# Kernel tuning notes

Measured on AMD Instinct MI355X. Metric: run time of the kernel, lower is better.

The kernel has to match this reference:

```python
import math
import jax, jax.numpy as jnp
import numpy as np


def _sinkhorn_attn(q, n):
    """Log-domain Sinkhorn-Knopp, eps=1, max_iter=1, uniform marginals.
    cost C = -q @ q^T, so M = (-C + u + v)/eps = S + u + v with S = q q^T.
    Returns transport plan pi = exp(S + u_i + v_j).  q: [B, n, d]."""
    S = jnp.einsum('bnd,bmd->bnm', q, q)            # [B, n, n]
    log_marg = -math.log(n)                          # log(1/n)
    u = log_marg - jax.nn.logsumexp(S, axis=-1)      # [B, n] row update
    v = log_marg - jax.nn.logsumexp(S + u[..., :, None], axis=-2)  # [B, n] col update
    return jnp.exp(S + u[..., :, None] + v[..., None, :])


def reference(x, row_embed, col_embed):
    # x: [B, d, H, W]; row_embed/col_embed: [len_embedding, d//2]
    B, d, H, W = x.shape
    # learned positional embedding: [H, W, d] -> [d, H, W]
    x_emb = col_embed[:W]                             # [W, F]
    y_emb = row_embed[:H]                             # [H, F]
    F = x_emb.shape[-1]
    pos = jnp.concatenate([
        jnp.broadcast_to(x_emb[None, :, :], (H, W, F)),
        jnp.broadcast_to(y_emb[:, None, :], (H, W, F)),
    ], axis=-1).transpose(2, 0, 1)                    # [d, H, W]
    x = x + pos[None]

    n = H * W
    xf = x.reshape(B, d, n).transpose(0, 2, 1)        # [B, n, d] = q = k = v (v unscaled)
    inv_sqrtV = 1.0 / math.sqrt(math.sqrt(d))         # d**-0.25 applied to q and k each
    attn = _sinkhorn_attn(xf * inv_sqrtV, n)          # [B, n, n]
    out = jnp.einsum('bnm,bmd->bnd', attn, xf)        # [B, n, d]
    return out.transpose(0, 2, 1).reshape(B, d, H, W)


def setup_inputs() -> dict:
    key = jax.random.key(0)
    k1, k2, k3 = jax.random.split(key, 3)
    B, d, H, W = 32, 512, 32, 32
    len_emb, F = 32, d // 2
    return {
        'x': jax.random.normal(k1, (B, d, H, W), dtype=jnp.float32),
        'row_embed': jax.random.uniform(k2, (len_emb, F), dtype=jnp.float32),
        'col_embed': jax.random.uniform(k3, (len_emb, F), dtype=jnp.float32),
    }
```

## Files before the change

kernel.cpp:

```cpp
#include <hip/hip_runtime.h>
#include <hip/hip_fp16.h>
#include <math.h>

typedef _Float16 f16;
typedef _Float16 f16x8 __attribute__((ext_vector_type(8)));
typedef _Float16 f16x4 __attribute__((ext_vector_type(4)));
typedef float f32x4 __attribute__((ext_vector_type(4)));

namespace {
constexpr int kB = 32, kD = 512, kN = 1024, kF = 256;
constexpr float kScale = 0.04419417382415922f;
constexpr float kLogMarg = -6.931471805599453f;
constexpr float kMarg = 1.f / 1024.f;
constexpr float kPScale = 16384.f;
constexpr float kPInv = 1.f / 16384.f;
constexpr int LDK = 72;
}

__global__ __launch_bounds__(256) void k_prep(
    const float* __restrict__ x, const float* __restrict__ re,
    const float* __restrict__ ce, f16* __restrict__ xf,
    f16* __restrict__ xfT, int b0) {
  __shared__ f16 T[64][68];
  const int lb = blockIdx.z;
  const int i0 = blockIdx.x * 64, c0 = blockIdx.y * 64;
  const int t = threadIdx.x;
  const int il = (t & 15) * 4;
  const int cl = t >> 4;
  const size_t xbase = ((size_t)(b0 + lb) * kD) * kN;
#pragma unroll
  for (int p = 0; p < 4; p++) {
    const int c = c0 + cl + 16 * p;
    const int i = i0 + il;
    const float4 xv = *(const float4*)(x + xbase + (size_t)c * kN + i);
    float4 pv;
    if (c < kF) {
      pv.x = ce[((i + 0) & 31) * kF + c];
      pv.y = ce[((i + 1) & 31) * kF + c];
      pv.z = ce[((i + 2) & 31) * kF + c];
      pv.w = ce[((i + 3) & 31) * kF + c];
    } else {
      const float r = re[(i >> 5) * kF + (c - kF)];
      pv.x = r; pv.y = r; pv.z = r; pv.w = r;
    }
    const f16 h0 = (f16)(xv.x + pv.x), h1 = (f16)(xv.y + pv.y);
    const f16 h2 = (f16)(xv.z + pv.z), h3 = (f16)(xv.w + pv.w);
    f16* dT = xfT + ((size_t)lb * kD + c) * kN + i;
    *(f16x4*)dT = (f16x4){h0, h1, h2, h3};
    T[cl + 16 * p][il + 0] = h0; T[cl + 16 * p][il + 1] = h1;
    T[cl + 16 * p][il + 2] = h2; T[cl + 16 * p][il + 3] = h3;
  }
  __syncthreads();
#pragma unroll
  for (int p = 0; p < 4; p++) {
    const int ir = cl + 16 * p;
    const int cc = il;
    const f16 h0 = T[cc + 0][ir], h1 = T[cc + 1][ir];
    const f16 h2 = T[cc + 2][ir], h3 = T[cc + 3][ir];
    f16* dF = xf + ((size_t)lb * kN + i0 + ir) * kD + c0 + cc;
    *(f16x4*)dF = (f16x4){h0, h1, h2, h3};
  }
}

__global__ __launch_bounds__(256) void k_gemm_s(
    const f16* __restrict__ xf, f16* __restrict__ S16,
    float* __restrict__ rp) {
  __shared__ f16 As[128][LDK];
  __shared__ f16 Bs[128][LDK];
  const int lb = blockIdx.z;
  const int i0 = blockIdx.y * 128, j0 = blockIdx.x * 128;
  const f16* base = xf + (size_t)lb * kN * kD;
  const int t = threadIdx.x;
  const int w = t >> 6, lane = t & 63;
  const int m_off = (w >> 1) * 64, n_off = (w & 1) * 64;
  const int quad = lane >> 4, l15 = lane & 15;
  const int sc = (t & 7) * 8;
  const int sr = t >> 3;
  f32x4 acc[4][4];
#pragma unroll
  for (int a = 0; a < 4; a++)
#pragma unroll
    for (int b = 0; b < 4; b++) acc[a][b] = (f32x4){0.f, 0.f, 0.f, 0.f};

  for (int k0 = 0; k0 < kD; k0 += 64) {
    f16x8 a[4], b[4];
#pragma unroll
    for (int p = 0; p < 4; p++) {
      a[p] = *(const f16x8*)(base + (size_t)(i0 + sr + 32 * p) * kD + k0 + sc);
      b[p] = *(const f16x8*)(base + (size_t)(j0 + sr + 32 * p) * kD + k0 + sc);
    }
    __syncthreads();
#pragma unroll
    for (int p = 0; p < 4; p++) {
      *(f16x8*)&As[sr + 32 * p][sc] = a[p];
      *(f16x8*)&Bs[sr + 32 * p][sc] = b[p];
    }
    __syncthreads();
#pragma unroll
    for (int kk = 0; kk < 64; kk += 32) {
      f16x8 af[4], bf[4];
#pragma unroll
      for (int q = 0; q < 4; q++)
        af[q] = *(const f16x8*)&As[m_off + 16 * q + l15][kk + quad * 8];
#pragma unroll
      for (int q = 0; q < 4; q++)
        bf[q] = *(const f16x8*)&Bs[n_off + 16 * q + l15][kk + quad * 8];
#pragma unroll
      for (int qa = 0; qa < 4; qa++)
#pragma unroll
        for (int qb = 0; qb < 4; qb++)
          acc[qa][qb] = __builtin_amdgcn_mfma_f32_16x16x32_f16(
              af[qa], bf[qb], acc[qa][qb], 0, 0, 0);
    }
  }
  f16* Sb = S16 + (size_t)lb * kN * kN;
  const int jt2 = blockIdx.x * 2 + (w & 1);
  float* rpb = rp + ((size_t)lb * 16 + jt2) * kN + i0 + m_off;
#pragma unroll
  for (int qa = 0; qa < 4; qa++) {
    const int i = i0 + m_off + 16 * qa + quad * 4;
    float rs[4] = {0.f, 0.f, 0.f, 0.f};
#pragma unroll
    for (int qb = 0; qb < 4; qb++) {
      const int j = j0 + n_off + 16 * qb + l15;
#pragma unroll
      for (int r = 0; r < 4; r++) {
        const f16 h = (f16)(acc[qa][qb][r] * kScale);
        Sb[(size_t)(i + r) * kN + j] = h;
        rs[r] += __expf((float)h);
      }
    }
#pragma unroll
    for (int r = 0; r < 4; r++) {
      float s = rs[r];
      s += __shfl_xor(s, 1);
      s += __shfl_xor(s, 2);
      s += __shfl_xor(s, 4);
      s += __shfl_xor(s, 8);
      if (l15 == 0) rpb[16 * qa + 4 * quad + r] = s;
    }
  }
}

__global__ __launch_bounds__(256) void k_u(
    const float* __restrict__ rp, float* __restrict__ u) {
  const int lb = blockIdx.y;
  const int i = blockIdx.x * 256 + threadIdx.x;
  const float* r = rp + (size_t)lb * 16 * kN + i;
  float s = 0.f;
#pragma unroll
  for (int t = 0; t < 16; t++) s += r[(size_t)t * kN];
  u[lb * kN + i] = kLogMarg - __logf(s);
}

__global__ __launch_bounds__(256) void k_cs(
    const f16* __restrict__ S16, const float* __restrict__ u,
    float* __restrict__ cp) {
  const int lb = blockIdx.z;
  const int seg = blockIdx.y;
  const int j = blockIdx.x * 256 + threadIdx.x;
  const f16* Sb = S16 + (size_t)lb * kN * kN + j;
  const float* ub = u + lb * kN + seg * 64;
  const size_t rbase = (size_t)(seg * 64) * kN;
  float s = 0.f;
#pragma unroll 4
  for (int r = 0; r < 64; r++)
    s += __expf((float)Sb[rbase + (size_t)r * kN] + ub[r]);
  cp[((size_t)lb * 16 + seg) * kN + j] = s;
}

__global__ __launch_bounds__(256) void k_v(
    const float* __restrict__ cp, float* __restrict__ ev) {
  const int lb = blockIdx.y;
  const int j = blockIdx.x * 256 + threadIdx.x;
  const float* c = cp + (size_t)lb * 16 * kN + j;
  float s = 0.f;
#pragma unroll
  for (int r = 0; r < 16; r++) s += c[(size_t)r * kN];
  ev[lb * kN + j] = kMarg / s;
}

__global__ __launch_bounds__(256) void k_pt(
    const f16* __restrict__ S16, const float* __restrict__ u,
    const float* __restrict__ ev, f16* __restrict__ t16) {
  const int row = blockIdx.x;
  const float ui = u[row];
  const f16* Sr = S16 + (size_t)row * kN;
  const float* evb = ev + (size_t)(row >> 10) * kN;
  f16* Tr = t16 + (size_t)row * kN;
  const int j = threadIdx.x * 4;
  const f16x4 s = *(const f16x4*)(Sr + j);
  const float4 e = *(const float4*)(evb + j);
  f16x4 o;
  o[0] = (f16)(__expf((float)s[0] + ui) * e.x * kPScale);
  o[1] = (f16)(__expf((float)s[1] + ui) * e.y * kPScale);
  o[2] = (f16)(__expf((float)s[2] + ui) * e.z * kPScale);
  o[3] = (f16)(__expf((float)s[3] + ui) * e.w * kPScale);
  *(f16x4*)(Tr + j) = o;
}

__global__ __launch_bounds__(256) void k_gemm_o(
    const f16* __restrict__ xfT, const f16* __restrict__ P,
    float* __restrict__ out, int b0) {
  __shared__ f16 As[128][LDK];
  __shared__ f16 Bs[128][LDK];
  const int lb = blockIdx.z;
  const int i0 = blockIdx.x * 128, c0 = blockIdx.y * 128;
  const f16* Ab = xfT + (size_t)lb * kD * kN;
  const f16* Bb = P + (size_t)lb * kN * kN;
  const int t = threadIdx.x;
  const int w = t >> 6, lane = t & 63;
  const int m_off = (w >> 1) * 64, n_off = (w & 1) * 64;
  const int quad = lane >> 4, l15 = lane & 15;
  const int sc = (t & 7) * 8;
  const int sr = t >> 3;
  f32x4 acc[4][4];
#pragma unroll
  for (int a = 0; a < 4; a++)
#pragma unroll
    for (int b = 0; b < 4; b++) acc[a][b] = (f32x4){0.f, 0.f, 0.f, 0.f};

  for (int k0 = 0; k0 < kN; k0 += 64) {
    f16x8 a[4], b[4];
#pragma unroll
    for (int p = 0; p < 4; p++) {
      a[p] = *(const f16x8*)(Ab + (size_t)(c0 + sr + 32 * p) * kN + k0 + sc);
      b[p] = *(const f16x8*)(Bb + (size_t)(i0 + sr + 32 * p) * kN + k0 + sc);
    }
    __syncthreads();
#pragma unroll
    for (int p = 0; p < 4; p++) {
      *(f16x8*)&As[sr + 32 * p][sc] = a[p];
      *(f16x8*)&Bs[sr + 32 * p][sc] = b[p];
    }
    __syncthreads();
#pragma unroll
    for (int kk = 0; kk < 64; kk += 32) {
      f16x8 af[4], bf[4];
#pragma unroll
      for (int q = 0; q < 4; q++)
        af[q] = *(const f16x8*)&As[m_off + 16 * q + l15][kk + quad * 8];
#pragma unroll
      for (int q = 0; q < 4; q++)
        bf[q] = *(const f16x8*)&Bs[n_off + 16 * q + l15][kk + quad * 8];
#pragma unroll
      for (int qa = 0; qa < 4; qa++)
#pragma unroll
        for (int qb = 0; qb < 4; qb++)
          acc[qa][qb] = __builtin_amdgcn_mfma_f32_16x16x32_f16(
              af[qa], bf[qb], acc[qa][qb], 0, 0, 0);
    }
  }
  float* ob = out + ((size_t)(b0 + lb) * kD) * kN;
#pragma unroll
  for (int qa = 0; qa < 4; qa++) {
    const int c = c0 + m_off + 16 * qa + quad * 4;
#pragma unroll
    for (int qb = 0; qb < 4; qb++) {
      const int i = i0 + n_off + 16 * qb + l15;
#pragma unroll
      for (int r = 0; r < 4; r++)
        ob[(size_t)(c + r) * kN + i] = acc[qa][qb][r] * kPInv;
    }
  }
}

extern "C" void kernel_launch(void* const* d_in, const int* in_sizes, int n_in,
                              void* d_out, int out_size, void* d_ws, size_t ws_size,
                              hipStream_t stream) {
  const float* x = (const float*)d_in[0];
  const float* re = (const float*)d_in[1];
  const float* ce = (const float*)d_in[2];
  float* out = (float*)d_out;

  char* wsb = (char*)d_ws;
  const size_t perb = 2097152ull + 1048576 + 1048576 + 2097152 +
                      4096 + 4096 + 65536 + 65536;
  int G = (int)(ws_size / perb);
  if (G >= 32) G = 32;
  else if (G >= 16) G = 16;
  else if (G >= 8) G = 8;
  else if (G >= 4) G = 4;
  else if (G < 1) G = 1;
  f16* S16 = (f16*)wsb;
  f16* xf = (f16*)(wsb + (size_t)G * 2097152);
  f16* xfT = (f16*)((char*)xf + (size_t)G * 1048576);
  f16* t16 = (f16*)((char*)xfT + (size_t)G * 1048576);
  float* u = (float*)((char*)t16 + (size_t)G * 2097152);
  float* ev = u + (size_t)G * kN;
  float* rp = ev + (size_t)G * kN;
  float* cp = rp + (size_t)G * 16 * kN;

  for (int b0 = 0; b0 < kB; b0 += G) {
    const int g = (kB - b0 < G) ? (kB - b0) : G;
    k_prep<<<dim3(16, 8, g), 256, 0, stream>>>(x, re, ce, xf, xfT, b0);
    k_gemm_s<<<dim3(8, 8, g), 256, 0, stream>>>(xf, S16, rp);
    k_u<<<dim3(4, g), 256, 0, stream>>>(rp, u);
    k_cs<<<dim3(4, 16, g), 256, 0, stream>>>(S16, u, cp);
    k_v<<<dim3(4, g), 256, 0, stream>>>(cp, ev);
    k_pt<<<g * kN, 256, 0, stream>>>(S16, u, ev, t16);
    k_gemm_o<<<dim3(8, 4, g), 256, 0, stream>>>(xfT, t16, out, b0);
  }
}
```

Before: 286.3 us.

## Load GEMM tiles directly into LDS with global_load_lds and XOR swizzle

Both GEMM kernels now fetch their A and B tiles straight from global memory into shared memory with the global_load_lds builtin. This bypasses the VGPR staging and separate LDS stores. The padded shared layout becomes a dense 128-byte row layout with an XOR swizzle on the 16-byte chunk index, applied to the source address and undone on the fragment reads, to avoid bank conflicts. The barrier after compute is kept, but loads are still not double-buffered, so load latency is not overlapped with MFMA work. The code relies on the wave-uniform LDS base plus per-lane 16-byte placement matching the precomputed swizzled source offsets.

```diff
diff --git a/kernel.cpp b/kernel.cpp
--- a/kernel.cpp
+++ b/kernel.cpp
@@ -14,7 +14,12 @@
 constexpr float kMarg = 1.f / 1024.f;
 constexpr float kPScale = 16384.f;
 constexpr float kPInv = 1.f / 16384.f;
-constexpr int LDK = 72;
+}
+
+__device__ __forceinline__ void gload16(const void* g, void* l) {
+  __builtin_amdgcn_global_load_lds(
+      (const __attribute__((address_space(1))) void*)g,
+      (__attribute__((address_space(3))) void*)l, 16, 0, 0);
 }
 
 __global__ __launch_bounds__(256) void k_prep(
@@ -65,46 +70,52 @@
 __global__ __launch_bounds__(256) void k_gemm_s(
     const f16* __restrict__ xf, f16* __restrict__ S16,
     float* __restrict__ rp) {
-  __shared__ f16 As[128][LDK];
-  __shared__ f16 Bs[128][LDK];
+  __shared__ char sm[32768];
   const int lb = blockIdx.z;
   const int i0 = blockIdx.y * 128, j0 = blockIdx.x * 128;
-  const f16* base = xf + (size_t)lb * kN * kD;
+  const char* base = (const char*)(xf + (size_t)lb * kN * kD);
   const int t = threadIdx.x;
   const int w = t >> 6, lane = t & 63;
   const int m_off = (w >> 1) * 64, n_off = (w & 1) * 64;
   const int quad = lane >> 4, l15 = lane & 15;
-  const int sc = (t & 7) * 8;
-  const int sr = t >> 3;
+  const int swz = (l15 & 7) << 4;
+
+  int srcA[4], srcB[4], ldsw[4];
+#pragma unroll
+  for (int p = 0; p < 4; p++) {
+    const int off = p * 4096 + w * 1024 + lane * 16;
+    const int r = off >> 7;
+    const int cb = (off & 127) ^ ((r & 7) << 4);
+    srcA[p] = (i0 + r) * (kD * 2) + cb;
+    srcB[p] = (j0 + r) * (kD * 2) + cb;
+    ldsw[p] = p * 4096 + w * 1024;
+  }
+
   f32x4 acc[4][4];
 #pragma unroll
   for (int a = 0; a < 4; a++)
 #pragma unroll
     for (int b = 0; b < 4; b++) acc[a][b] = (f32x4){0.f, 0.f, 0.f, 0.f};
 
-  for (int k0 = 0; k0 < kD; k0 += 64) {
-    f16x8 a[4], b[4];
-#pragma unroll
-    for (int p = 0; p < 4; p++) {
-      a[p] = *(const f16x8*)(base + (size_t)(i0 + sr + 32 * p) * kD + k0 + sc);
-      b[p] = *(const f16x8*)(base + (size_t)(j0 + sr + 32 * p) * kD + k0 + sc);
-    }
+  for (int k0b = 0; k0b < kD * 2; k0b += 128) {
+#pragma unroll
+    for (int p = 0; p < 4; p++)
+      gload16(base + srcA[p] + k0b, sm + ldsw[p]);
+#pragma unroll
+    for (int p = 0; p < 4; p++)
+      gload16(base + srcB[p] + k0b, sm + 16384 + ldsw[p]);
     __syncthreads();
 #pragma unroll
-    for (int p = 0; p < 4; p++) {
-      *(f16x8*)&As[sr + 32 * p][sc] = a[p];
-      *(f16x8*)&Bs[sr + 32 * p][sc] = b[p];
-    }
-    __syncthreads();
-#pragma unroll
-    for (int kk = 0; kk < 64; kk += 32) {
+    for (int kk = 0; kk < 2; kk++) {
       f16x8 af[4], bf[4];
 #pragma unroll
       for (int q = 0; q < 4; q++)
-        af[q] = *(const f16x8*)&As[m_off + 16 * q + l15][kk + quad * 8];
+        af[q] = *(const f16x8*)(sm + (m_off + 16 * q + l15) * 128 +
+                                ((kk * 64 + quad * 16) ^ swz));
 #pragma unroll
       for (int q = 0; q < 4; q++)
-        bf[q] = *(const f16x8*)&Bs[n_off + 16 * q + l15][kk + quad * 8];
+        bf[q] = *(const f16x8*)(sm + 16384 + (n_off + 16 * q + l15) * 128 +
+                                ((kk * 64 + quad * 16) ^ swz));
 #pragma unroll
       for (int qa = 0; qa < 4; qa++)
 #pragma unroll
@@ -112,7 +123,9 @@
           acc[qa][qb] = __builtin_amdgcn_mfma_f32_16x16x32_f16(
               af[qa], bf[qb], acc[qa][qb], 0, 0, 0);
     }
-  }
+    __syncthreads();
+  }
+
   f16* Sb = S16 + (size_t)lb * kN * kN;
   const int jt2 = blockIdx.x * 2 + (w & 1);
   float* rpb = rp + ((size_t)lb * 16 + jt2) * kN + i0 + m_off;
@@ -202,47 +215,53 @@
 __global__ __launch_bounds__(256) void k_gemm_o(
     const f16* __restrict__ xfT, const f16* __restrict__ P,
     float* __restrict__ out, int b0) {
-  __shared__ f16 As[128][LDK];
-  __shared__ f16 Bs[128][LDK];
+  __shared__ char sm[32768];
   const int lb = blockIdx.z;
   const int i0 = blockIdx.x * 128, c0 = blockIdx.y * 128;
-  const f16* Ab = xfT + (size_t)lb * kD * kN;
-  const f16* Bb = P + (size_t)lb * kN * kN;
+  const char* Ab = (const char*)(xfT + (size_t)lb * kD * kN);
+  const char* Bb = (const char*)(P + (size_t)lb * kN * kN);
   const int t = threadIdx.x;
   const int w = t >> 6, lane = t & 63;
   const int m_off = (w >> 1) * 64, n_off = (w & 1) * 64;
   const int quad = lane >> 4, l15 = lane & 15;
-  const int sc = (t & 7) * 8;
-  const int sr = t >> 3;
+  const int swz = (l15 & 7) << 4;
+
+  int srcA[4], srcB[4], ldsw[4];
+#pragma unroll
+  for (int p = 0; p < 4; p++) {
+    const int off = p * 4096 + w * 1024 + lane * 16;
+    const int r = off >> 7;
+    const int cb = (off & 127) ^ ((r & 7) << 4);
+    srcA[p] = (c0 + r) * (kN * 2) + cb;
+    srcB[p] = (i0 + r) * (kN * 2) + cb;
+    ldsw[p] = p * 4096 + w * 1024;
+  }
+
   f32x4 acc[4][4];
 #pragma unroll
   for (int a = 0; a < 4; a++)
 #pragma unroll
     for (int b = 0; b < 4; b++) acc[a][b] = (f32x4){0.f, 0.f, 0.f, 0.f};
 
-  for (int k0 = 0; k0 < kN; k0 += 64) {
-    f16x8 a[4], b[4];
-#pragma unroll
-    for (int p = 0; p < 4; p++) {
-      a[p] = *(const f16x8*)(Ab + (size_t)(c0 + sr + 32 * p) * kN + k0 + sc);
-      b[p] = *(const f16x8*)(Bb + (size_t)(i0 + sr + 32 * p) * kN + k0 + sc);
-    }
+  for (int k0b = 0; k0b < kN * 2; k0b += 128) {
+#pragma unroll
+    for (int p = 0; p < 4; p++)
+      gload16(Ab + srcA[p] + k0b, sm + ldsw[p]);
+#pragma unroll
+    for (int p = 0; p < 4; p++)
+      gload16(Bb + srcB[p] + k0b, sm + 16384 + ldsw[p]);
     __syncthreads();
 #pragma unroll
-    for (int p = 0; p < 4; p++) {
-      *(f16x8*)&As[sr + 32 * p][sc] = a[p];
-      *(f16x8*)&Bs[sr + 32 * p][sc] = b[p];
-    }
-    __syncthreads();
-#pragma unroll
-    for (int kk = 0; kk < 64; kk += 32) {
+    for (int kk = 0; kk < 2; kk++) {
       f16x8 af[4], bf[4];
 #pragma unroll
       for (int q = 0; q < 4; q++)
-        af[q] = *(const f16x8*)&As[m_off + 16 * q + l15][kk + quad * 8];
+        af[q] = *(const f16x8*)(sm + (m_off + 16 * q + l15) * 128 +
+                                ((kk * 64 + quad * 16) ^ swz));
 #pragma unroll
       for (int q = 0; q < 4; q++)
-        bf[q] = *(const f16x8*)&Bs[n_off + 16 * q + l15][kk + quad * 8];
+        bf[q] = *(const f16x8*)(sm + 16384 + (n_off + 16 * q + l15) * 128 +
+                                ((kk * 64 + quad * 16) ^ swz));
 #pragma unroll
       for (int qa = 0; qa < 4; qa++)
 #pragma unroll
@@ -250,7 +269,9 @@
           acc[qa][qb] = __builtin_amdgcn_mfma_f32_16x16x32_f16(
               af[qa], bf[qb], acc[qa][qb], 0, 0, 0);
     }
-  }
+    __syncthreads();
+  }
+
   float* ob = out + ((size_t)(b0 + lb) * kD) * kN;
 #pragma unroll
   for (int qa = 0; qa < 4; qa++) {
```

After: 280.5 us. 1.02x faster.
